# Kernel optimization log

Measured on AMD Instinct MI355X. Metric: run time of the kernel, lower is better.

## Reference

```python
import jax, jax.numpy as jnp
import numpy as np

EPS = 1e-6
K_HOPS = 2  # SGConv K


def setup_inputs() -> dict:
    key = jax.random.key(0)
    k1, k2, k3, k4 = jax.random.split(key, 4)
    B, Kk, C, T = 32, 8, 64, 250
    E, H = 4096, 128
    x = jax.random.normal(k1, (B, Kk, C, T), dtype=jnp.float32)
    edge_index = jax.random.randint(k2, (2, E), 0, C, dtype=jnp.int64)
    edge_weights = jax.random.uniform(k3, (E,), dtype=jnp.float32)
    W = jax.random.normal(k4, (H, Kk * T), dtype=jnp.float32) * 0.02
    b = jnp.zeros((H,), dtype=jnp.float32)
    return {"x": x, "edge_index": edge_index, "edge_weights": edge_weights, "W": W, "b": b}


def reference(x, edge_index, edge_weights, W, b):
    B, Kk, C, T = x.shape
    N = C  # nodes
    x = x.reshape(B, N, Kk * T)  # (B, N, F)

    # clamp non-positive edge weights to epsilon (mirrors in-place .data clamp)
    w = jnp.where(edge_weights <= 0, EPS, edge_weights)

    # gcn_norm with self loops (fill value 1.0)
    src, dst = edge_index[0], edge_index[1]
    loop = jnp.arange(N, dtype=edge_index.dtype)
    src = jnp.concatenate([src, loop])
    dst = jnp.concatenate([dst, loop])
    w = jnp.concatenate([w, jnp.ones((N,), w.dtype)])
    deg = jnp.zeros((N,), w.dtype).at[dst].add(w)
    dinv = jnp.where(deg > 0, deg ** -0.5, jnp.zeros_like(deg))
    norm = dinv[src] * w * dinv[dst]  # (E+N,)

    # K hops of gather -> weight -> scatter-add aggregation
    for _ in range(K_HOPS):
        msg = x[:, src, :] * norm[None, :, None]        # (B, E+N, F)
        x = jnp.zeros_like(x).at[:, dst, :].add(msg)    # (B, N, F)

    # final linear: y = x @ W^T + b
    return jnp.einsum('bnf,hf->bnh', x, W) + b
```

## Files before the change

kernel.cpp:

```cpp
#include <hip/hip_runtime.h>
#include <hip/hip_bf16.h>

#define EPSW 1e-6f

typedef __attribute__((ext_vector_type(4))) float floatx4;
typedef __attribute__((ext_vector_type(8))) short shortx8;

__device__ __forceinline__ shortx8 pack8(floatx4 a, floatx4 b) {
    union { shortx8 v; unsigned int u[4]; } r;
    const unsigned a0 = __float_as_uint(a.x) + 0x8000u, a1 = __float_as_uint(a.y) + 0x8000u;
    const unsigned a2 = __float_as_uint(a.z) + 0x8000u, a3 = __float_as_uint(a.w) + 0x8000u;
    const unsigned b0 = __float_as_uint(b.x) + 0x8000u, b1 = __float_as_uint(b.y) + 0x8000u;
    const unsigned b2 = __float_as_uint(b.z) + 0x8000u, b3 = __float_as_uint(b.w) + 0x8000u;
    r.u[0] = __builtin_amdgcn_perm(a1, a0, 0x07060302u);
    r.u[1] = __builtin_amdgcn_perm(a3, a2, 0x07060302u);
    r.u[2] = __builtin_amdgcn_perm(b1, b0, 0x07060302u);
    r.u[3] = __builtin_amdgcn_perm(b3, b2, 0x07060302u);
    return r.v;
}

#define XSTR 136

__global__ __launch_bounds__(512, 2) void fused_all(
        const float* __restrict__ x, const float* __restrict__ W,
        const int* __restrict__ ei, const float* __restrict__ ew,
        const float* __restrict__ bias, float* __restrict__ y) {
    __shared__ __align__(16) unsigned short smem[29952];
    unsigned short* xs0 = smem;
    unsigned short* xs1 = smem + 8704;
    unsigned short* ww0 = smem + 17408;
    unsigned short* ww1 = smem + 19584;
    float* Ms = (float*)(smem + 21760);
    float* A    = (float*)smem;
    float* deg  = (float*)xs1;
    float* dinv = deg + 64;
    float(*zs)[17] = (float(*)[17])smem;

    const int t   = threadIdx.x;
    const int bid = blockIdx.x;
    const int b   = bid & 31;
    const int ht  = bid >> 5;

    {
        if (t < 64) deg[t] = 1.0f;
        for (int i = t; i < 4096; i += 512) A[i] = 0.0f;
        __syncthreads();
        const int* srcp = ei;
        const int* dstp = ei + 4096;
#pragma unroll
        for (int i = 0; i < 8; ++i) {
            const int e = i * 512 + t;
            float w = ew[e];
            w = (w <= 0.0f) ? EPSW : w;
            atomicAdd(&deg[dstp[e]], w);
        }
        __syncthreads();
        if (t < 64) dinv[t] = 1.0f / sqrtf(deg[t]);
        __syncthreads();
#pragma unroll
        for (int i = 0; i < 8; ++i) {
            const int e = i * 512 + t;
            float w = ew[e];
            w = (w <= 0.0f) ? EPSW : w;
            const int s = srcp[e], d = dstp[e];
            atomicAdd(&A[d * 64 + s], dinv[s] * w * dinv[d]);
        }
        if (t < 64) atomicAdd(&A[t * 64 + t], dinv[t] * dinv[t]);
        __syncthreads();
#pragma unroll
        for (int i = 0; i < 8; ++i) {
            const int idx = i * 512 + t;
            const int n = idx >> 6, c = idx & 63;
            float s = 0.0f;
#pragma unroll 8
            for (int k = 0; k < 64; ++k) s += A[n * 64 + k] * A[k * 64 + c];
            Ms[c * 64 + n] = s;
        }
        __syncthreads();
    }

    const int wave = t >> 6, lane = t & 63;
    const int m = lane & 15, q = lane >> 4;
    const int rt = wave & 3, kh = wave >> 2;

    const float* xb = x + (size_t)b * 64 * 2000;
    const float* Wb = W + (size_t)ht * 16 * 2000;

    const int xr0 = t >> 4,         xk0 = (t & 15) * 8;
    const int xr1 = (t + 512) >> 4, xk1 = xk0;
    const int wr  = t >> 4,         wk  = (t & 15) * 8;

    floatx4 px0a, px0b, px1a, px1b, pwa, pwb;
    const floatx4 zero4 = (floatx4){0.f, 0.f, 0.f, 0.f};

#define LOAD_CHUNK(kbase)                                                     \
    {                                                                         \
        const int k0 = (kbase) + xk0;                                         \
        if (k0 < 2000) {                                                      \
            px0a = *(const floatx4*)(xb + (size_t)xr0 * 2000 + k0);           \
            px0b = *(const floatx4*)(xb + (size_t)xr0 * 2000 + k0 + 4);       \
            px1a = *(const floatx4*)(xb + (size_t)xr1 * 2000 + k0);           \
            px1b = *(const floatx4*)(xb + (size_t)xr1 * 2000 + k0 + 4);       \
        } else { px0a = zero4; px0b = zero4; px1a = zero4; px1b = zero4; }    \
        if (t < 256) {                                                        \
            const int kw = (kbase) + wk;                                      \
            if (kw < 2000) {                                                  \
                pwa = *(const floatx4*)(Wb + (size_t)wr * 2000 + kw);         \
                pwb = *(const floatx4*)(Wb + (size_t)wr * 2000 + kw + 4);     \
            } else { pwa = zero4; pwb = zero4; }                              \
        }                                                                     \
    }

    LOAD_CHUNK(0);

    floatx4 acc0 = zero4, acc1 = zero4;
    for (int c = 0; c < 16; ++c) {
        unsigned short* xsb = (c & 1) ? xs1 : xs0;
        unsigned short* wwb = (c & 1) ? ww1 : ww0;
        *(shortx8*)&xsb[xr0 * XSTR + xk0] = pack8(px0a, px0b);
        *(shortx8*)&xsb[xr1 * XSTR + xk1] = pack8(px1a, px1b);
        if (t < 256) *(shortx8*)&wwb[wr * XSTR + wk] = pack8(pwa, pwb);
        __syncthreads();
        if (c < 15) LOAD_CHUNK((c + 1) * 128);
        const unsigned short* xrow = &xsb[(rt * 16 + m) * XSTR + kh * 64 + q * 8];
        const unsigned short* wrow = &wwb[m * XSTR + kh * 64 + q * 8];
        const shortx8 a0 = *(const shortx8*)xrow;
        const shortx8 b0 = *(const shortx8*)wrow;
        const shortx8 a1 = *(const shortx8*)(xrow + 32);
        const shortx8 b1 = *(const shortx8*)(wrow + 32);
        acc0 = __builtin_amdgcn_mfma_f32_16x16x32_bf16(a0, b0, acc0, 0, 0, 0);
        acc1 = __builtin_amdgcn_mfma_f32_16x16x32_bf16(a1, b1, acc1, 0, 0, 0);
        __syncthreads();
    }
    acc0 += acc1;

    if (kh == 0) {
#pragma unroll
        for (int v = 0; v < 4; ++v) zs[rt * 16 + q * 4 + v][m] = acc0[v];
    }
    __syncthreads();
    if (kh == 1) {
#pragma unroll
        for (int v = 0; v < 4; ++v) zs[rt * 16 + q * 4 + v][m] += acc0[v];
    }
    __syncthreads();
    {
        const int n0 = t >> 4;
        const int h  = t & 15;
        const float bv = bias[ht * 16 + h];
        float s0 = bv, s1 = bv;
#pragma unroll
        for (int mm = 0; mm < 64; ++mm) {
            const float zv = zs[mm][h];
            s0 += Ms[mm * 64 + n0]      * zv;
            s1 += Ms[mm * 64 + n0 + 32] * zv;
        }
        float* yp = y + (size_t)b * 8192 + ht * 16 + h;
        yp[(size_t)n0 * 128]        = s0;
        yp[(size_t)(n0 + 32) * 128] = s1;
    }
}

extern "C" void kernel_launch(void* const* d_in, const int* in_sizes, int n_in,
                              void* d_out, int out_size, void* d_ws, size_t ws_size,
                              hipStream_t stream) {
    const float* x    = (const float*)d_in[0];
    const int*   ei   = (const int*)d_in[1];
    const float* ew   = (const float*)d_in[2];
    const float* W    = (const float*)d_in[3];
    const float* bias = (const float*)d_in[4];
    float* y = (float*)d_out;

    fused_all<<<256, 512, 0, stream>>>(x, W, ei, ew, bias, y);
}
```

Before: 102.5 us.

## Compute propagation matrix once in a separate kernel instead of per block

Splits the graph-normalization and A² computation into a prep kernel of 16 blocks that writes M to workspace. The main GEMM kernel then just loads M from global memory, so the 256 blocks no longer each redo the atomics and the 64x64x64 matmul. The launch bounds are relaxed and the LDS row stride changes from 136 to 132. In exchange it adds a second kernel launch with a dependency between the two, and the new stride may change LDS bank-conflict behaviour.

After: 107.6 us. 5.0% more time.

```diff
diff --git a/kernel.cpp b/kernel.cpp
--- a/kernel.cpp
+++ b/kernel.cpp
@@ -19,69 +19,75 @@
     return r.v;
 }
 
-#define XSTR 136
+__global__ __launch_bounds__(256) void prep_M(const int* __restrict__ ei,
+                                              const float* __restrict__ ew,
+                                              float* __restrict__ Mt) {
+    __shared__ float A[4096];
+    __shared__ float deg[64];
+    __shared__ float dinv[64];
+    const int bid = blockIdx.x;
+    const int t   = threadIdx.x;
+    if (t < 64) deg[t] = 1.0f;
+    for (int i = t; i < 4096; i += 256) A[i] = 0.0f;
+    __syncthreads();
+    const int* srcp = ei;
+    const int* dstp = ei + 4096;
+#pragma unroll
+    for (int i = 0; i < 16; ++i) {
+        const int e = i * 256 + t;
+        float w = ew[e];
+        w = (w <= 0.0f) ? EPSW : w;
+        atomicAdd(&deg[dstp[e]], w);
+    }
+    __syncthreads();
+    if (t < 64) dinv[t] = 1.0f / sqrtf(deg[t]);
+    __syncthreads();
+#pragma unroll
+    for (int i = 0; i < 16; ++i) {
+        const int e = i * 256 + t;
+        float w = ew[e];
+        w = (w <= 0.0f) ? EPSW : w;
+        const int s = srcp[e], d = dstp[e];
+        atomicAdd(&A[d * 64 + s], dinv[s] * w * dinv[d]);
+    }
+    if (t < 64) atomicAdd(&A[t * 64 + t], dinv[t] * dinv[t]);
+    __syncthreads();
+    const int c = bid * 4 + (t >> 6);
+    const int n = t & 63;
+    float s = 0.0f;
+#pragma unroll 8
+    for (int k = 0; k < 64; ++k) s += A[n * 64 + k] * A[k * 64 + c];
+    Mt[c * 64 + n] = s;
+}
 
-__global__ __launch_bounds__(512, 2) void fused_all(
+#define XSTR 132
+
+__global__ __launch_bounds__(512) void gemm_fused(
         const float* __restrict__ x, const float* __restrict__ W,
-        const int* __restrict__ ei, const float* __restrict__ ew,
-        const float* __restrict__ bias, float* __restrict__ y) {
-    __shared__ __align__(16) unsigned short smem[29952];
+        const float* __restrict__ Mt, const float* __restrict__ bias,
+        float* __restrict__ y) {
+    __shared__ __align__(16) unsigned short smem[29312];
     unsigned short* xs0 = smem;
-    unsigned short* xs1 = smem + 8704;
-    unsigned short* ww0 = smem + 17408;
-    unsigned short* ww1 = smem + 19584;
-    float* Ms = (float*)(smem + 21760);
-    float* A    = (float*)smem;
-    float* deg  = (float*)xs1;
-    float* dinv = deg + 64;
+    unsigned short* xs1 = smem + 8448;
+    unsigned short* ww0 = smem + 16896;
+    unsigned short* ww1 = smem + 19008;
+    float* Ms = (float*)(smem + 21120);
     float(*zs)[17] = (float(*)[17])smem;
 
     const int t   = threadIdx.x;
     const int bid = blockIdx.x;
     const int b   = bid & 31;
     const int ht  = bid >> 5;
-
-    {
-        if (t < 64) deg[t] = 1.0f;
-        for (int i = t; i < 4096; i += 512) A[i] = 0.0f;
-        __syncthreads();
-        const int* srcp = ei;
-        const int* dstp = ei + 4096;
-#pragma unroll
-        for (int i = 0; i < 8; ++i) {
-            const int e = i * 512 + t;
-            float w = ew[e];
-            w = (w <= 0.0f) ? EPSW : w;
-            atomicAdd(&deg[dstp[e]], w);
-        }
-        __syncthreads();
-        if (t < 64) dinv[t] = 1.0f / sqrtf(deg[t]);
-        __syncthreads();
-#pragma unroll
-        for (int i = 0; i < 8; ++i) {
-            const int e = i * 512 + t;
-            float w = ew[e];
-            w = (w <= 0.0f) ? EPSW : w;
-            const int s = srcp[e], d = dstp[e];
-            atomicAdd(&A[d * 64 + s], dinv[s] * w * dinv[d]);
-        }
-        if (t < 64) atomicAdd(&A[t * 64 + t], dinv[t] * dinv[t]);
-        __syncthreads();
-#pragma unroll
-        for (int i = 0; i < 8; ++i) {
-            const int idx = i * 512 + t;
-            const int n = idx >> 6, c = idx & 63;
-            float s = 0.0f;
-#pragma unroll 8
-            for (int k = 0; k < 64; ++k) s += A[n * 64 + k] * A[k * 64 + c];
-            Ms[c * 64 + n] = s;
-        }
-        __syncthreads();
-    }
-
     const int wave = t >> 6, lane = t & 63;
     const int m = lane & 15, q = lane >> 4;
     const int rt = wave & 3, kh = wave >> 2;
+
+    {
+        const floatx4* Mg4 = (const floatx4*)Mt;
+        floatx4* Ms4 = (floatx4*)Ms;
+        Ms4[t]       = Mg4[t];
+        Ms4[t + 512] = Mg4[t + 512];
+    }
 
     const float* xb = x + (size_t)b * 64 * 2000;
     const float* Wb = W + (size_t)ht * 16 * 2000;
@@ -171,5 +177,8 @@
     const float* bias = (const float*)d_in[4];
     float* y = (float*)d_out;
 
-    fused_all<<<256, 512, 0, stream>>>(x, W, ei, ew, bias, y);
+    float* Mt = (float*)d_ws;
+
+    prep_M<<<16, 256, 0, stream>>>(ei, ew, Mt);
+    gemm_fused<<<256, 512, 0, stream>>>(x, W, Mt, bias, y);
 }
```
